# Kernel optimization log

Measured on AMD Instinct MI355X. Metric: run time of the kernel, lower is better.

## Reference

```python
import jax, jax.numpy as jnp
import numpy as np

B, N, DIN, DINNER, DOUT, W = 4, 8192, 512, 512, 512, 128


def setup_inputs() -> dict:
    key = jax.random.key(0)
    k1, k2, k3 = jax.random.split(key, 3)
    x = jax.random.normal(k1, (B, N, DIN), jnp.float32)
    # torch Linear weights: (out_features, in_features)
    w_qkv = jax.random.normal(k2, (3 * DINNER, DIN), jnp.float32) * (DIN ** -0.5)
    w_out = jax.random.normal(k3, (DOUT, DINNER), jnp.float32) * (DINNER ** -0.5)
    b_out = jnp.zeros((DOUT,), jnp.float32)
    return {"x": x, "w_qkv": w_qkv, "w_out": w_out, "b_out": b_out}


def reference(x, w_qkv, w_out, b_out):
    b, n, _ = x.shape
    w = W
    scale = DINNER ** -0.5
    pad = (-n) % w  # pad_to_multiple along seq dim (static)
    xp = jnp.pad(x, ((0, 0), (0, pad), (0, 0)))
    qkv = jnp.einsum('bnd,ed->bne', xp, w_qkv)  # to_qkv, no bias
    q, k, v = jnp.split(qkv, 3, axis=-1)
    win = lambda t: t.reshape(b, -1, w, DINNER)  # b (w n) d -> b w n d
    q, k, v = win(q), win(k), win(v)
    # prepend one zero bucket to k, then overlap prev/current windows.
    kp = jnp.pad(k, ((0, 0), (1, 0), (0, 0), (0, 0)))
    k2 = jnp.concatenate((kp[:, :-1], kp[:, 1:]), axis=2)  # (b, nb, 2w, d)
    # NOTE: source bug replicated — v is also built from k, not v.
    v2 = jnp.concatenate((kp[:, :-1], kp[:, 1:]), axis=2)
    sim = jnp.einsum('bwid,bwjd->bwij', q, k2) * scale  # (b, nb, w, 2w)
    i, j = w, 2 * w
    mask = jnp.triu(jnp.ones((i, j), bool), j - i + 1)
    sim = jnp.where(mask, -jnp.finfo(sim.dtype).max, sim)
    attn = jax.nn.softmax(sim, axis=-1)
    out = jnp.einsum('bwij,bwjd->bwid', attn, v2)
    out = out.reshape(b, -1, DINNER)[:, :n]
    return jnp.einsum('bnd,od->bno', out, w_out) + b_out
```

## Files before the change

kernel.cpp:

```cpp
#include <hip/hip_runtime.h>
#include <cstdint>
#include <cstddef>

typedef float f32x4 __attribute__((ext_vector_type(4)));
typedef short s16x8 __attribute__((ext_vector_type(8)));
typedef short s16x4 __attribute__((ext_vector_type(4)));

#define MFMA_BF16(a, b, c) __builtin_amdgcn_mfma_f32_16x16x32_bf16((a), (b), (c), 0, 0, 0)

#define GLD16(g, l)                                                            \
  __builtin_amdgcn_global_load_lds(                                            \
      (const __attribute__((address_space(1))) void*)(g),                      \
      (__attribute__((address_space(3))) void*)(l), 16, 0, 0)

__device__ __forceinline__ unsigned short f2bf(float f) {
  unsigned int u = __float_as_uint(f);
  u += 0x7FFFu + ((u >> 16) & 1u);
  return (unsigned short)(u >> 16);
}

__device__ __forceinline__ s16x8 cvt8(const float* __restrict__ src) {
  const float4 f0 = *(const float4*)src;
  const float4 f1 = *(const float4*)(src + 4);
  s16x8 h;
  h[0] = (short)f2bf(f0.x); h[1] = (short)f2bf(f0.y);
  h[2] = (short)f2bf(f0.z); h[3] = (short)f2bf(f0.w);
  h[4] = (short)f2bf(f1.x); h[5] = (short)f2bf(f1.y);
  h[6] = (short)f2bf(f1.z); h[7] = (short)f2bf(f1.w);
  return h;
}

#define XN 16777216
#define WQN 524288
__global__ __launch_bounds__(256)
void cvt_bf16(const float* __restrict__ x, const float* __restrict__ wqkv,
              const float* __restrict__ wout, unsigned short* __restrict__ xb,
              unsigned short* __restrict__ wb, unsigned short* __restrict__ wob) {
  const size_t i = (size_t)(blockIdx.x * 256 + threadIdx.x) * 8;
  const float* src;
  unsigned short* dst;
  if (i < XN) { src = x + i; dst = xb + i; }
  else if (i < XN + WQN) { src = wqkv + (i - XN); dst = wb + (i - XN); }
  else { src = wout + (i - XN - WQN); dst = wob + (i - XN - WQN); }
  *(s16x8*)dst = cvt8(src);
}

__global__ __launch_bounds__(256)
void gemm_qk(const unsigned short* __restrict__ xb, const unsigned short* __restrict__ wb,
             unsigned short* __restrict__ Q, unsigned short* __restrict__ K) {
  __shared__ unsigned short As[128 * 64];
  __shared__ unsigned short Bs[128 * 64];
  const int t = threadIdx.x, lane = t & 63, wid = t >> 6;
  const int wm = wid >> 1, wn = wid & 1;
  const int nl = lane & 15, quad = lane >> 4;
  const int sub = lane >> 3, lblk = (lane & 7) ^ sub;
  const int l = blockIdx.x;
  const int xcd = l & 7, g = l >> 3;
  const int mt = (g >> 3) * 8 + xcd, nt = g & 7;
  const int m0 = mt * 128, n0 = nt * 128;

  const f32x4 zero = {0.f, 0.f, 0.f, 0.f};
  f32x4 acc[4][4];
#pragma unroll
  for (int i = 0; i < 4; ++i)
#pragma unroll
    for (int j = 0; j < 4; ++j) acc[i][j] = zero;

  const unsigned short* gX = xb + (size_t)(m0 + wid * 32 + sub) * 512 + lblk * 8;
  const unsigned short* gW = wb + (size_t)(n0 + wid * 32 + sub) * 512 + lblk * 8;

  for (int kc = 0; kc < 512; kc += 64) {
#pragma unroll
    for (int ii = 0; ii < 4; ++ii) {
      GLD16(gW + kc + (size_t)(ii * 8) * 512, &As[(wid * 32 + ii * 8) * 64]);
      GLD16(gX + kc + (size_t)(ii * 8) * 512, &Bs[(wid * 32 + ii * 8) * 64]);
    }
    __syncthreads();
#pragma unroll
    for (int ks = 0; ks < 2; ++ks) {
      s16x8 af[4], bf[4];
#pragma unroll
      for (int i = 0; i < 4; ++i)
        af[i] = *(const s16x8*)&As[(wm * 64 + i * 16 + nl) * 64 +
                                   (((ks * 4 + quad) ^ (nl & 7)) * 8)];
#pragma unroll
      for (int j = 0; j < 4; ++j)
        bf[j] = *(const s16x8*)&Bs[(wn * 64 + j * 16 + nl) * 64 +
                                   (((ks * 4 + quad) ^ (nl & 7)) * 8)];
#pragma unroll
      for (int i = 0; i < 4; ++i)
#pragma unroll
        for (int j = 0; j < 4; ++j) acc[i][j] = MFMA_BF16(af[i], bf[j], acc[i][j]);
    }
    __syncthreads();
  }
#pragma unroll
  for (int i = 0; i < 4; ++i) {
    const int n = n0 + wm * 64 + i * 16 + quad * 4;
    unsigned short* base = (n < 512 ? Q : K);
    const int nn = n & 511;
#pragma unroll
    for (int j = 0; j < 4; ++j) {
      const int m = m0 + wn * 64 + j * 16 + nl;
      s16x4 h;
#pragma unroll
      for (int r = 0; r < 4; ++r) h[r] = (short)f2bf(acc[i][j][r]);
      *(s16x4*)&base[(size_t)m * 512 + nn] = h;
    }
  }
}

__global__ __launch_bounds__(256)
void gemm_kwt(const unsigned short* __restrict__ K, const unsigned short* __restrict__ wob,
              unsigned short* __restrict__ KWT) {
  __shared__ unsigned short As[128 * 64];
  __shared__ unsigned short Bs[128 * 64];
  const int t = threadIdx.x, lane = t & 63, wid = t >> 6;
  const int wm = wid >> 1, wn = wid & 1;
  const int nl = lane & 15, quad = lane >> 4;
  const int sub = lane >> 3, lblk = (lane & 7) ^ sub;
  const int l = blockIdx.x;
  const int xcd = l & 7, g = l >> 3;
  const int mt = (g >> 2) * 8 + xcd, nt = g & 3;
  const int m0 = mt * 128, n0 = nt * 128;

  const f32x4 zero = {0.f, 0.f, 0.f, 0.f};
  f32x4 acc[4][4];
#pragma unroll
  for (int i = 0; i < 4; ++i)
#pragma unroll
    for (int j = 0; j < 4; ++j) acc[i][j] = zero;

  const unsigned short* gA = K + (size_t)(m0 + wid * 32 + sub) * 512 + lblk * 8;
  const unsigned short* gB = wob + (size_t)(n0 + wid * 32 + sub) * 512 + lblk * 8;

  for (int kc = 0; kc < 512; kc += 64) {
#pragma unroll
    for (int ii = 0; ii < 4; ++ii) {
      GLD16(gA + kc + (size_t)(ii * 8) * 512, &As[(wid * 32 + ii * 8) * 64]);
      GLD16(gB + kc + (size_t)(ii * 8) * 512, &Bs[(wid * 32 + ii * 8) * 64]);
    }
    __syncthreads();
#pragma unroll
    for (int ks = 0; ks < 2; ++ks) {
      s16x8 af[4], bf[4];
#pragma unroll
      for (int i = 0; i < 4; ++i)
        af[i] = *(const s16x8*)&As[(wm * 64 + i * 16 + nl) * 64 +
                                   (((ks * 4 + quad) ^ (nl & 7)) * 8)];
#pragma unroll
      for (int j = 0; j < 4; ++j)
        bf[j] = *(const s16x8*)&Bs[(wn * 64 + j * 16 + nl) * 64 +
                                   (((ks * 4 + quad) ^ (nl & 7)) * 8)];
#pragma unroll
      for (int i = 0; i < 4; ++i)
#pragma unroll
        for (int j = 0; j < 4; ++j) acc[i][j] = MFMA_BF16(af[i], bf[j], acc[i][j]);
    }
    __syncthreads();
  }
#pragma unroll
  for (int i = 0; i < 4; ++i) {
    const int ms = m0 + wm * 64 + i * 16 + quad * 4;
    const int b = ms >> 13, ns = ms & 8191;
#pragma unroll
    for (int j = 0; j < 4; ++j) {
      const int o = n0 + wn * 64 + j * 16 + nl;
      s16x4 h;
#pragma unroll
      for (int r = 0; r < 4; ++r) h[r] = (short)f2bf(acc[i][j][r]);
      *(s16x4*)&KWT[(size_t)(b * 512 + o) * 8192 + ns] = h;
    }
  }
}

__global__ __launch_bounds__(256)
void attn64(const unsigned short* __restrict__ Q, const unsigned short* __restrict__ K,
            const unsigned short* __restrict__ KWT, const float* __restrict__ bias,
            float* __restrict__ out) {
  __shared__ char smem[49152];
  unsigned short* Qs = (unsigned short*)smem;
  unsigned short* Ks = (unsigned short*)(smem + 8192);
  unsigned short* Ps = (unsigned short*)smem;
  unsigned short* Bs2 = (unsigned short*)(smem + 32768);
  __shared__ float redm[256];
  __shared__ float reds[256];
  const int t = threadIdx.x, lane = t & 63, wid = t >> 6;
  const int wn = wid;
  const int nl = lane & 15, quad = lane >> 4;
  const int sub = lane >> 3, lblk = (lane & 7) ^ sub;
  const int bx = blockIdx.x;
  const int xcd = bx & 7, half = (bx >> 3) & 1, g = bx >> 4;
  const int wb = g * 8 + xcd, b = wb >> 6, w = wb & 63;

  const f32x4 zero = {0.f, 0.f, 0.f, 0.f};
  f32x4 acc[4][4];
#pragma unroll
  for (int i = 0; i < 4; ++i)
#pragma unroll
    for (int j = 0; j < 4; ++j) acc[i][j] = zero;

  const unsigned short* Qb = Q + (size_t)(b * 8192 + w * 128 + half * 64) * 512;
  const unsigned short* Kb = K + (size_t)(b * 8192) * 512;

  for (int kc = 0; kc < 512; kc += 64) {
#pragma unroll
    for (int ii = 0; ii < 2; ++ii)
      GLD16(Qb + (size_t)(wid * 16 + ii * 8 + sub) * 512 + kc + lblk * 8,
            &Qs[(wid * 16 + ii * 8) * 64]);
#pragma unroll
    for (int ii = 0; ii < 8; ++ii) {
      int sq = w * 128 - 128 + wid * 64 + ii * 8 + sub;
      if (sq < 0) sq = 0;
      GLD16(Kb + (size_t)sq * 512 + kc + lblk * 8, &Ks[(wid * 64 + ii * 8) * 64]);
    }
    __syncthreads();
#pragma unroll
    for (int ks = 0; ks < 2; ++ks) {
      s16x8 af[4], bf[4];
#pragma unroll
      for (int i = 0; i < 4; ++i)
        af[i] = *(const s16x8*)&Qs[(i * 16 + nl) * 64 +
                                   (((ks * 4 + quad) ^ (nl & 7)) * 8)];
#pragma unroll
      for (int j = 0; j < 4; ++j)
        bf[j] = *(const s16x8*)&Ks[(wn * 64 + j * 16 + nl) * 64 +
                                   (((ks * 4 + quad) ^ (nl & 7)) * 8)];
#pragma unroll
      for (int i = 0; i < 4; ++i)
#pragma unroll
        for (int j = 0; j < 4; ++j) acc[i][j] = MFMA_BF16(af[i], bf[j], acc[i][j]);
    }
    __syncthreads();
  }

  const float scale = 0.04419417382415922f;
  float rmax[4][4];
#pragma unroll
  for (int i = 0; i < 4; ++i) {
#pragma unroll
    for (int r = 0; r < 4; ++r) {
      const int qrow = half * 64 + i * 16 + quad * 4 + r;
      float mx = -3.4e38f;
#pragma unroll
      for (int j = 0; j < 4; ++j) {
        const int col = wn * 64 + j * 16 + nl;
        float v = acc[i][j][r] * scale;
        if (col >= 128 && col - 128 > qrow) v = -3.0e38f;
        if (w == 0 && col < 128) v = 0.0f;
        acc[i][j][r] = v;
        mx = fmaxf(mx, v);
      }
      rmax[i][r] = mx;
    }
  }
#pragma unroll
  for (int off = 1; off < 16; off <<= 1)
#pragma unroll
    for (int i = 0; i < 4; ++i)
#pragma unroll
      for (int r = 0; r < 4; ++r)
        rmax[i][r] = fmaxf(rmax[i][r], __shfl_xor(rmax[i][r], off, 64));
  if (nl == 0) {
#pragma unroll
    for (int i = 0; i < 4; ++i)
#pragma unroll
      for (int r = 0; r < 4; ++r)
        redm[(i * 16 + quad * 4 + r) * 4 + wn] = rmax[i][r];
  }
  __syncthreads();
  float rsum[4][4];
#pragma unroll
  for (int i = 0; i < 4; ++i) {
#pragma unroll
    for (int r = 0; r < 4; ++r) {
      const f32x4 mv = *(const f32x4*)&redm[(i * 16 + quad * 4 + r) * 4];
      const float m = fmaxf(fmaxf(mv[0], mv[1]), fmaxf(mv[2], mv[3]));
      float s = 0.f;
#pragma unroll
      for (int j = 0; j < 4; ++j) {
        const float p = __expf(acc[i][j][r] - m);
        acc[i][j][r] = p;
        s += p;
      }
      rsum[i][r] = s;
    }
  }
#pragma unroll
  for (int off = 1; off < 16; off <<= 1)
#pragma unroll
    for (int i = 0; i < 4; ++i)
#pragma unroll
      for (int r = 0; r < 4; ++r) rsum[i][r] += __shfl_xor(rsum[i][r], off, 64);
  if (nl == 0) {
#pragma unroll
    for (int i = 0; i < 4; ++i)
#pragma unroll
      for (int r = 0; r < 4; ++r)
        reds[(i * 16 + quad * 4 + r) * 4 + wn] = rsum[i][r];
  }
  __syncthreads();
#pragma unroll
  for (int i = 0; i < 4; ++i) {
#pragma unroll
    for (int r = 0; r < 4; ++r) {
      const int row = i * 16 + quad * 4 + r;
      const f32x4 sv = *(const f32x4*)&reds[row * 4];
      const float inv = 1.0f / (sv[0] + sv[1] + sv[2] + sv[3]);
#pragma unroll
      for (int j = 0; j < 4; ++j) {
        const int col = wn * 64 + j * 16 + nl;
        float pv = acc[i][j][r] * inv;
        if (w == 0 && col < 128) pv = 0.0f;
        const int cb = col >> 3;
        Ps[row * 256 + (((cb ^ (row & 7)) << 3) | (col & 7))] = f2bf(pv);
      }
    }
  }
  __syncthreads();

  const int seqbase = w * 128 - 128;
#pragma unroll 1
  for (int och = 0; och < 4; ++och) {
    f32x4 acc2[4][2];
#pragma unroll
    for (int i = 0; i < 4; ++i)
#pragma unroll
      for (int j = 0; j < 2; ++j) acc2[i][j] = zero;
#pragma unroll 1
    for (int kch = 0; kch < 4; ++kch) {
      int sq = seqbase + kch * 64 + lblk * 8;
      if (sq < 0) sq = 0;
#pragma unroll
      for (int ii = 0; ii < 4; ++ii) {
        const int orow = och * 128 + wid * 32 + ii * 8 + sub;
        GLD16(KWT + (size_t)(b * 512 + orow) * 8192 + sq, &Bs2[(wid * 32 + ii * 8) * 64]);
      }
      __syncthreads();
#pragma unroll
      for (int ks = 0; ks < 2; ++ks) {
        const int kb = kch * 8 + ks * 4 + quad;
        s16x8 af[4], bf[2];
#pragma unroll
        for (int i = 0; i < 4; ++i)
          af[i] = *(const s16x8*)&Ps[(i * 16 + nl) * 256 + ((kb ^ (nl & 7)) << 3)];
#pragma unroll
        for (int j = 0; j < 2; ++j)
          bf[j] = *(const s16x8*)&Bs2[(wn * 32 + j * 16 + nl) * 64 +
                                      (((ks * 4 + quad) ^ (nl & 7)) * 8)];
#pragma unroll
        for (int i = 0; i < 4; ++i)
#pragma unroll
          for (int j = 0; j < 2; ++j) acc2[i][j] = MFMA_BF16(af[i], bf[j], acc2[i][j]);
      }
      __syncthreads();
    }
#pragma unroll
    for (int i = 0; i < 4; ++i) {
      const int seq = w * 128 + half * 64 + i * 16 + quad * 4;
      float* dst = out + (size_t)(b * 8192 + seq) * 512;
#pragma unroll
      for (int j = 0; j < 2; ++j) {
        const int o = och * 128 + wn * 32 + j * 16 + nl;
        const float bo = bias[o];
#pragma unroll
        for (int r = 0; r < 4; ++r) dst[(size_t)r * 512 + o] = acc2[i][j][r] + bo;
      }
    }
  }
}

extern "C" void kernel_launch(void* const* d_in, const int* in_sizes, int n_in,
                              void* d_out, int out_size, void* d_ws, size_t ws_size,
                              hipStream_t stream) {
  const float* x = (const float*)d_in[0];
  const float* w_qkv = (const float*)d_in[1];
  const float* w_out = (const float*)d_in[2];
  const float* b_out = (const float*)d_in[3];
  float* out = (float*)d_out;

  char* ws = (char*)d_ws;
  unsigned short* Q = (unsigned short*)ws;
  unsigned short* K = (unsigned short*)(ws + (size_t)33554432);
  unsigned short* xb = (unsigned short*)(ws + (size_t)67108864);
  unsigned short* KWT = (unsigned short*)(ws + (size_t)67108864);
  unsigned short* wb = (unsigned short*)(ws + (size_t)100663296);
  unsigned short* wob = (unsigned short*)(ws + (size_t)100663296 + 1048576);

  cvt_bf16<<<dim3(8576), dim3(256), 0, stream>>>(x, w_qkv, w_out, xb, wb, wob);
  gemm_qk<<<dim3(2048), dim3(256), 0, stream>>>(xb, wb, Q, K);
  gemm_kwt<<<dim3(1024), dim3(256), 0, stream>>>(K, wob, KWT);
  attn64<<<dim3(512), dim3(256), 0, stream>>>(Q, K, KWT, b_out, out);
}
```

Baseline: 234.8 us.

## Load attention MFMA operands directly from global memory instead of LDS staging

```diff
diff --git a/kernel.cpp b/kernel.cpp
--- a/kernel.cpp
+++ b/kernel.cpp
@@ -178,17 +178,12 @@
 void attn64(const unsigned short* __restrict__ Q, const unsigned short* __restrict__ K,
             const unsigned short* __restrict__ KWT, const float* __restrict__ bias,
             float* __restrict__ out) {
-  __shared__ char smem[49152];
-  unsigned short* Qs = (unsigned short*)smem;
-  unsigned short* Ks = (unsigned short*)(smem + 8192);
-  unsigned short* Ps = (unsigned short*)smem;
-  unsigned short* Bs2 = (unsigned short*)(smem + 32768);
+  __shared__ unsigned short Ps[64 * 256];
   __shared__ float redm[256];
   __shared__ float reds[256];
   const int t = threadIdx.x, lane = t & 63, wid = t >> 6;
   const int wn = wid;
   const int nl = lane & 15, quad = lane >> 4;
-  const int sub = lane >> 3, lblk = (lane & 7) ^ sub;
   const int bx = blockIdx.x;
   const int xcd = bx & 7, half = (bx >> 3) & 1, g = bx >> 4;
   const int wb = g * 8 + xcd, b = wb >> 6, w = wb & 63;
@@ -203,35 +198,34 @@
   const unsigned short* Qb = Q + (size_t)(b * 8192 + w * 128 + half * 64) * 512;
   const unsigned short* Kb = K + (size_t)(b * 8192) * 512;
 
+  const unsigned short* qptr[4];
+  const unsigned short* kptr[4];
+#pragma unroll
+  for (int i = 0; i < 4; ++i) qptr[i] = Qb + (size_t)(i * 16 + nl) * 512;
+#pragma unroll
+  for (int j = 0; j < 4; ++j) {
+    int seq = w * 128 - 128 + wn * 64 + j * 16 + nl;
+    if (seq < 0) seq = 0;
+    kptr[j] = Kb + (size_t)seq * 512;
+  }
+
+#pragma unroll 2
   for (int kc = 0; kc < 512; kc += 64) {
 #pragma unroll
-    for (int ii = 0; ii < 2; ++ii)
-      GLD16(Qb + (size_t)(wid * 16 + ii * 8 + sub) * 512 + kc + lblk * 8,
-            &Qs[(wid * 16 + ii * 8) * 64]);
-#pragma unroll
-    for (int ii = 0; ii < 8; ++ii) {
-      int sq = w * 128 - 128 + wid * 64 + ii * 8 + sub;
-      if (sq < 0) sq = 0;
-      GLD16(Kb + (size_t)sq * 512 + kc + lblk * 8, &Ks[(wid * 64 + ii * 8) * 64]);
-    }
-    __syncthreads();
-#pragma unroll
     for (int ks = 0; ks < 2; ++ks) {
+      const int off = kc + (ks * 4 + quad) * 8;
       s16x8 af[4], bf[4];
 #pragma unroll
-      for (int i = 0; i < 4; ++i)
-        af[i] = *(const s16x8*)&Qs[(i * 16 + nl) * 64 +
-                                   (((ks * 4 + quad) ^ (nl & 7)) * 8)];
-#pragma unroll
-      for (int j = 0; j < 4; ++j)
-        bf[j] = *(const s16x8*)&Ks[(wn * 64 + j * 16 + nl) * 64 +
-                                   (((ks * 4 + quad) ^ (nl & 7)) * 8)];
+      for (int i = 0; i < 4; ++i) af[i] = *(const s16x8*)(qptr[i] + off);
+#pragma unroll
+      for (int j = 0; j < 4; ++j) bf[j] = *(const s16x8*)(kptr[j] + off);
+      __builtin_amdgcn_s_setprio(1);
 #pragma unroll
       for (int i = 0; i < 4; ++i)
 #pragma unroll
         for (int j = 0; j < 4; ++j) acc[i][j] = MFMA_BF16(af[i], bf[j], acc[i][j]);
-    }
-    __syncthreads();
+      __builtin_amdgcn_s_setprio(0);
+    }
   }
 
   const float scale = 0.04419417382415922f;
@@ -327,33 +321,30 @@
     for (int i = 0; i < 4; ++i)
 #pragma unroll
       for (int j = 0; j < 2; ++j) acc2[i][j] = zero;
-#pragma unroll 1
+    const unsigned short* bp0 =
+        KWT + (size_t)(b * 512 + och * 128 + wn * 32 + nl) * 8192;
+    const unsigned short* bp1 = bp0 + (size_t)16 * 8192;
+#pragma unroll
     for (int kch = 0; kch < 4; ++kch) {
-      int sq = seqbase + kch * 64 + lblk * 8;
-      if (sq < 0) sq = 0;
-#pragma unroll
-      for (int ii = 0; ii < 4; ++ii) {
-        const int orow = och * 128 + wid * 32 + ii * 8 + sub;
-        GLD16(KWT + (size_t)(b * 512 + orow) * 8192 + sq, &Bs2[(wid * 32 + ii * 8) * 64]);
-      }
-      __syncthreads();
 #pragma unroll
       for (int ks = 0; ks < 2; ++ks) {
+        int sq = seqbase + kch * 64 + (ks * 4 + quad) * 8;
+        if (sq < 0) sq = 0;
         const int kb = kch * 8 + ks * 4 + quad;
         s16x8 af[4], bf[2];
 #pragma unroll
         for (int i = 0; i < 4; ++i)
           af[i] = *(const s16x8*)&Ps[(i * 16 + nl) * 256 + ((kb ^ (nl & 7)) << 3)];
-#pragma unroll
-        for (int j = 0; j < 2; ++j)
-          bf[j] = *(const s16x8*)&Bs2[(wn * 32 + j * 16 + nl) * 64 +
-                                      (((ks * 4 + quad) ^ (nl & 7)) * 8)];
-#pragma unroll
-        for (int i = 0; i < 4; ++i)
-#pragma unroll
-          for (int j = 0; j < 2; ++j) acc2[i][j] = MFMA_BF16(af[i], bf[j], acc2[i][j]);
-      }
-      __syncthreads();
+        bf[0] = *(const s16x8*)(bp0 + sq);
+        bf[1] = *(const s16x8*)(bp1 + sq);
+        __builtin_amdgcn_s_setprio(1);
+#pragma unroll
+        for (int i = 0; i < 4; ++i) {
+          acc2[i][0] = MFMA_BF16(af[i], bf[0], acc2[i][0]);
+          acc2[i][1] = MFMA_BF16(af[i], bf[1], acc2[i][1]);
+        }
+        __builtin_amdgcn_s_setprio(0);
+      }
     }
 #pragma unroll
     for (int i = 0; i < 4; ++i) {
```

New measurement: 255.3 us. 1.09x slower.
